# Kernel tuning notes

Hardware: AMD Instinct MI355X
Metric: run time of the kernel (lower is better)

## Reference

```python
import jax, jax.numpy as jnp
import numpy as np
import math

B, S, D, H = 2, 2048, 1024, 16
DK = D // H
EPS = 1e-6
TEMPERATURE = 1.0


def layernorm(x, a2, b2):
    # torch LayerNorm-variant: unbiased std (ddof=1), eps added to std
    mean = jnp.mean(x, axis=-1, keepdims=True)
    std = jnp.std(x, axis=-1, keepdims=True, ddof=1)
    return a2 * (x - mean) / (std + EPS) + b2


def setup_inputs() -> dict:
    key = jax.random.key(0)
    ks = jax.random.split(key, 12)
    scale = 1.0 / math.sqrt(D)
    inp = {
        "k": jax.random.normal(ks[0], (B, S, D), jnp.float32),
        "q": jax.random.normal(ks[1], (B, S, D), jnp.float32),
        "v": jax.random.normal(ks[2], (B, S, D), jnp.float32),
        "mask": jax.random.randint(ks[3], (B, S, S), 0, 2, jnp.int32),
        "Wq": jax.random.normal(ks[4], (D, D), jnp.float32) * scale,
        "bq": jnp.zeros((D,), jnp.float32),
        "Wk": jax.random.normal(ks[5], (D, D), jnp.float32) * scale,
        "bk": jnp.zeros((D,), jnp.float32),
        "Wv": jax.random.normal(ks[6], (D, D), jnp.float32) * scale,
        "bv": jnp.zeros((D,), jnp.float32),
        "Wo": jax.random.normal(ks[7], (D, D), jnp.float32) * scale,
        "bo": jnp.zeros((D,), jnp.float32),
        "a2": jnp.ones((D,), jnp.float32),
        "b2": jnp.zeros((D,), jnp.float32),
    }
    return inp


def reference(k, q, v, mask, Wq, bq, Wk, bk, Wv, bv, Wo, bo, a2, b2):
    # pre-norm all three streams
    kn = layernorm(k, a2, b2)
    qn = layernorm(q, a2, b2)
    vn = layernorm(v, a2, b2)
    # NOTE original quirk: linears[0](k)->query, linears[1](q)->key, linears[2](v)->value
    def proj(x, W, b):  # [B,S,D] -> [B,H,S,DK]
        y = x @ W + b
        return y.reshape(B, S, H, DK).transpose(0, 2, 1, 3)
    query = proj(kn, Wq, bq)
    key_ = proj(qn, Wk, bk)
    value = proj(vn, Wv, bv)
    scores = jnp.einsum('bhqd,bhkd->bhqk', query, key_) / math.sqrt(DK)
    scores = jnp.where(mask[:, None, :, :] == 0, jnp.float32(-1e9), scores)
    p_attn = jax.nn.softmax(scores * TEMPERATURE, axis=-1)
    x = jnp.einsum('bhqk,bhkd->bhqd', p_attn, value)
    x = x.transpose(0, 2, 1, 3).reshape(B, S, D)
    return x @ Wo + bo + vn  # residual adds normalized v
```

## Files before the change

kernel.cpp:

```cpp
#include <hip/hip_runtime.h>
#include <hip/hip_bf16.h>

#define B_  2
#define S_  2048
#define D_  1024
#define H_  16
#define DK_ 64
#define M_  4096

using bf16x8 = __attribute__((ext_vector_type(8))) __bf16;
using f32x4  = __attribute__((ext_vector_type(4))) float;

typedef __attribute__((address_space(1))) void gvoid;
typedef __attribute__((address_space(3))) void lvoid;

__device__ __forceinline__ void gload_lds16(const void* g, void* l) {
  __builtin_amdgcn_global_load_lds((gvoid*)g, (lvoid*)l, 16, 0, 0);
}

__device__ __forceinline__ f32x4 mfma16(bf16x8 a, bf16x8 b, f32x4 c) {
  return __builtin_amdgcn_mfma_f32_16x16x32_bf16(a, b, c, 0, 0, 0);
}

__device__ __forceinline__ int swz64(int row, int ce) {
  return row * 64 + ((((ce >> 3) ^ (row & 7)) << 3) | (ce & 7));
}

__global__ __launch_bounds__(256) void ln3_kernel(
    const float* __restrict__ kin, const float* __restrict__ qin,
    const float* __restrict__ vin,
    const float* __restrict__ a2, const float* __restrict__ b2,
    __hip_bfloat16* __restrict__ kn, __hip_bfloat16* __restrict__ qn,
    __hip_bfloat16* __restrict__ vnb, float* __restrict__ vnf)
{
  const int row = blockIdx.x;
  const int st  = blockIdx.y;
  const float* src = (st == 0) ? kin : (st == 1) ? qin : vin;
  const int t = threadIdx.x;
  const size_t base = (size_t)row * D_;

  float4 x = *(const float4*)(src + base + t * 4);
  float s  = x.x + x.y + x.z + x.w;
  float s2 = x.x * x.x + x.y * x.y + x.z * x.z + x.w * x.w;
  #pragma unroll
  for (int off = 32; off >= 1; off >>= 1) {
    s  += __shfl_down(s,  off, 64);
    s2 += __shfl_down(s2, off, 64);
  }
  __shared__ float red[4][2];
  __shared__ float stats[2];
  const int wid = t >> 6, lane = t & 63;
  if (lane == 0) { red[wid][0] = s; red[wid][1] = s2; }
  __syncthreads();
  if (t == 0) {
    float S  = red[0][0] + red[1][0] + red[2][0] + red[3][0];
    float S2 = red[0][1] + red[1][1] + red[2][1] + red[3][1];
    float mean = S * (1.0f / D_);
    float var  = fmaxf((S2 - S * mean) * (1.0f / (D_ - 1)), 0.0f);
    stats[0] = mean;
    stats[1] = 1.0f / (sqrtf(var) + 1e-6f);
  }
  __syncthreads();
  const float mean = stats[0], inv = stats[1];
  float4 ga = *(const float4*)(a2 + t * 4);
  float4 gb = *(const float4*)(b2 + t * 4);
  float o0 = ga.x * (x.x - mean) * inv + gb.x;
  float o1 = ga.y * (x.y - mean) * inv + gb.y;
  float o2 = ga.z * (x.z - mean) * inv + gb.z;
  float o3 = ga.w * (x.w - mean) * inv + gb.w;
  __hip_bfloat16* dst = (st == 0) ? kn : (st == 1) ? qn : vnb;
  union { __hip_bfloat16 h[4]; ushort4 u; } pk;
  pk.h[0] = __float2bfloat16(o0); pk.h[1] = __float2bfloat16(o1);
  pk.h[2] = __float2bfloat16(o2); pk.h[3] = __float2bfloat16(o3);
  *reinterpret_cast<ushort4*>((unsigned short*)dst + base + t * 4) = pk.u;
  if (st == 2) {
    float4 of = make_float4(o0, o1, o2, o3);
    *reinterpret_cast<float4*>(vnf + base + t * 4) = of;
  }
}

__global__ __launch_bounds__(256) void pack_mask_kernel(
    const int* __restrict__ mask, unsigned int* __restrict__ bits)
{
  const int w = blockIdx.x * 256 + threadIdx.x;
  const int* src = mask + (size_t)w * 32;
  unsigned int acc = 0;
  #pragma unroll
  for (int j = 0; j < 32; j += 4) {
    int4 t = *(const int4*)(src + j);
    acc |= (t.x != 0 ? 1u : 0u) << (j + 0);
    acc |= (t.y != 0 ? 1u : 0u) << (j + 1);
    acc |= (t.z != 0 ? 1u : 0u) << (j + 2);
    acc |= (t.w != 0 ? 1u : 0u) << (j + 3);
  }
  bits[w] = acc;
}

__global__ __launch_bounds__(256) void wt_cast_kernel(
    const float* __restrict__ W0, const float* __restrict__ W1,
    const float* __restrict__ W2, const float* __restrict__ W3,
    __hip_bfloat16* __restrict__ T0, __hip_bfloat16* __restrict__ T1,
    __hip_bfloat16* __restrict__ T2, __hip_bfloat16* __restrict__ T3)
{
  const int z = blockIdx.z;
  const float* W = (z == 0) ? W0 : (z == 1) ? W1 : (z == 2) ? W2 : W3;
  __hip_bfloat16* T = (z == 0) ? T0 : (z == 1) ? T1 : (z == 2) ? T2 : T3;
  __shared__ float tile[32][33];
  const int k0 = blockIdx.y * 32, n0 = blockIdx.x * 32;
  const int tx = threadIdx.x & 31, ty = threadIdx.x >> 5;
  #pragma unroll
  for (int i = ty; i < 32; i += 8)
    tile[i][tx] = W[(size_t)(k0 + i) * D_ + n0 + tx];
  __syncthreads();
  #pragma unroll
  for (int i = ty; i < 32; i += 8)
    T[(size_t)(n0 + i) * D_ + k0 + tx] = __float2bfloat16(tile[tx][i]);
}

__global__ __launch_bounds__(256) void proj3_kernel(
    const __hip_bfloat16* __restrict__ kn, const __hip_bfloat16* __restrict__ qn,
    const __hip_bfloat16* __restrict__ vnb,
    const __hip_bfloat16* __restrict__ Wqt, const __hip_bfloat16* __restrict__ Wkt,
    const __hip_bfloat16* __restrict__ Wvt,
    const float* __restrict__ bq, const float* __restrict__ bk,
    const float* __restrict__ bv,
    __hip_bfloat16* __restrict__ Qb, __hip_bfloat16* __restrict__ Kb,
    __hip_bfloat16* __restrict__ Vtb)
{
  const int z = blockIdx.z;
  const __hip_bfloat16* A  = (z == 0) ? kn  : (z == 1) ? qn  : vnb;
  const __hip_bfloat16* Wt = (z == 0) ? Wqt : (z == 1) ? Wkt : Wvt;
  const float* bias = (z == 0) ? bq : (z == 1) ? bk : bv;
  const float scale = (z == 0) ? 0.125f : 1.0f;

  __shared__ __hip_bfloat16 As[128 * 32];
  __shared__ __hip_bfloat16 Bs[128 * 32];
  const int n0 = blockIdx.x * 128;
  const int m0 = blockIdx.y * 128;
  const int tid = threadIdx.x;
  const int wid = tid >> 6, lane = tid & 63;
  const int wm = wid >> 1, wn = wid & 1;
  const int srow = lane >> 2;
  const int scol = (lane & 3) * 8;
  const int fr = lane & 15, fk8 = (lane >> 4) * 8, fq = lane >> 4;

  f32x4 acc[4][4] = {};

  for (int kt = 0; kt < D_ / 32; ++kt) {
    const int k0 = kt * 32;
    #pragma unroll
    for (int p = 0; p < 2; ++p) {
      const int r0 = 32 * wid + 16 * p;
      gload_lds16(A  + (size_t)(m0 + r0 + srow) * D_ + k0 + scol, &As[r0 * 32]);
      gload_lds16(Wt + (size_t)(n0 + r0 + srow) * D_ + k0 + scol, &Bs[r0 * 32]);
    }
    __syncthreads();
    bf16x8 af[4], bfr[4];
    #pragma unroll
    for (int i = 0; i < 4; ++i)
      af[i] = *(const bf16x8*)&As[(64 * wm + 16 * i + fr) * 32 + fk8];
    #pragma unroll
    for (int j = 0; j < 4; ++j)
      bfr[j] = *(const bf16x8*)&Bs[(64 * wn + 16 * j + fr) * 32 + fk8];
    #pragma unroll
    for (int i = 0; i < 4; ++i)
      #pragma unroll
      for (int j = 0; j < 4; ++j)
        acc[i][j] = mfma16(af[i], bfr[j], acc[i][j]);
    __syncthreads();
  }

  #pragma unroll
  for (int i = 0; i < 4; ++i) {
    #pragma unroll
    for (int j = 0; j < 4; ++j) {
      const int n = n0 + 64 * wn + 16 * j + fr;
      const float bn = bias[n];
      const int h = n >> 6, d = n & (DK_ - 1);
      #pragma unroll
      for (int r = 0; r < 4; ++r) {
        const int m = m0 + 64 * wm + 16 * i + 4 * fq + r;
        const int b = m >> 11, sl = m & (S_ - 1);
        const float val = (acc[i][j][r] + bn) * scale;
        if (z < 2) {
          __hip_bfloat16* dst = (z == 0) ? Qb : Kb;
          dst[((size_t)(b * H_ + h) * S_ + sl) * DK_ + d] = __float2bfloat16(val);
        } else {
          Vtb[((size_t)(b * H_ + h) * DK_ + d) * S_ + sl] = __float2bfloat16(val);
        }
      }
    }
  }
}

__global__ __launch_bounds__(256) void gemm_out_kernel(
    const __hip_bfloat16* __restrict__ A,
    const __hip_bfloat16* __restrict__ Wt,
    const float* __restrict__ bias,
    const float* __restrict__ residf,
    float* __restrict__ dst)
{
  __shared__ __hip_bfloat16 As[128 * 32];
  __shared__ __hip_bfloat16 Bs[128 * 32];
  const int n0 = blockIdx.x * 128;
  const int m0 = blockIdx.y * 128;
  const int tid = threadIdx.x;
  const int wid = tid >> 6, lane = tid & 63;
  const int wm = wid >> 1, wn = wid & 1;
  const int srow = lane >> 2;
  const int scol = (lane & 3) * 8;
  const int fr = lane & 15, fk8 = (lane >> 4) * 8, fq = lane >> 4;

  f32x4 acc[4][4] = {};

  for (int kt = 0; kt < D_ / 32; ++kt) {
    const int k0 = kt * 32;
    #pragma unroll
    for (int p = 0; p < 2; ++p) {
      const int r0 = 32 * wid + 16 * p;
      gload_lds16(A  + (size_t)(m0 + r0 + srow) * D_ + k0 + scol, &As[r0 * 32]);
      gload_lds16(Wt + (size_t)(n0 + r0 + srow) * D_ + k0 + scol, &Bs[r0 * 32]);
    }
    __syncthreads();
    bf16x8 af[4], bfr[4];
    #pragma unroll
    for (int i = 0; i < 4; ++i)
      af[i] = *(const bf16x8*)&As[(64 * wm + 16 * i + fr) * 32 + fk8];
    #pragma unroll
    for (int j = 0; j < 4; ++j)
      bfr[j] = *(const bf16x8*)&Bs[(64 * wn + 16 * j + fr) * 32 + fk8];
    #pragma unroll
    for (int i = 0; i < 4; ++i)
      #pragma unroll
      for (int j = 0; j < 4; ++j)
        acc[i][j] = mfma16(af[i], bfr[j], acc[i][j]);
    __syncthreads();
  }

  #pragma unroll
  for (int i = 0; i < 4; ++i) {
    #pragma unroll
    for (int j = 0; j < 4; ++j) {
      const int n = n0 + 64 * wn + 16 * j + fr;
      const float bn = bias[n];
      #pragma unroll
      for (int r = 0; r < 4; ++r) {
        const int m = m0 + 64 * wm + 16 * i + 4 * fq + r;
        dst[(size_t)m * D_ + n] =
            acc[i][j][r] + bn + residf[(size_t)m * D_ + n];
      }
    }
  }
}

__global__ __launch_bounds__(256) void attn_kernel(
    const __hip_bfloat16* __restrict__ Qb,
    const __hip_bfloat16* __restrict__ Kb,
    const __hip_bfloat16* __restrict__ Vtb,
    const unsigned int* __restrict__ mbits,
    __hip_bfloat16* __restrict__ Ob)
{
  __shared__ __hip_bfloat16 Ks[64 * 64];
  __shared__ __hip_bfloat16 Vs[64 * 64];
  __shared__ __hip_bfloat16 Ps[4][16 * 64];

  const int q0 = blockIdx.x * 64;
  const int bh = blockIdx.y;
  const int b = bh >> 4;
  const int h = bh & 15;
  const int tid = threadIdx.x, wid = tid >> 6, lane = tid & 63;
  const __hip_bfloat16* qp = Qb  + (size_t)bh * S_ * DK_;
  const __hip_bfloat16* kp = Kb  + (size_t)bh * S_ * DK_;
  const __hip_bfloat16* vp = Vtb + (size_t)bh * DK_ * S_;

  const int srow = lane >> 3;
  const int scol = ((lane & 7) ^ (lane >> 3)) << 3;
  const int fr = lane & 15, fq = lane >> 4, fk8 = fq * 8;

  const unsigned int* mrow = mbits + (size_t)b * S_ * (S_ / 32)
                           + (size_t)(q0 + 16 * wid + 4 * fq) * (S_ / 32);

  bf16x8 aq[2];
  #pragma unroll
  for (int ks = 0; ks < 2; ++ks)
    aq[ks] = *(const bf16x8*)(qp + (size_t)(q0 + 16 * wid + fr) * DK_
                                 + ks * 32 + fk8);

  float lrun[4] = {0.0f, 0.0f, 0.0f, 0.0f};
  f32x4 acc[4] = {};

  for (int kt = 0; kt < S_ / 64; ++kt) {
    const int k0 = kt * 64;
    #pragma unroll
    for (int p = 0; p < 2; ++p) {
      const int r0 = 16 * wid + 8 * p;
      gload_lds16(kp + (size_t)(k0 + r0 + srow) * DK_ + scol, &Ks[r0 * 64]);
      gload_lds16(vp + (size_t)(r0 + srow) * S_ + k0 + scol,  &Vs[r0 * 64]);
    }
    __syncthreads();

    f32x4 sf[4] = {};
    __builtin_amdgcn_s_setprio(1);
    #pragma unroll
    for (int ks = 0; ks < 2; ++ks) {
      #pragma unroll
      for (int ni = 0; ni < 4; ++ni) {
        const bf16x8 bk = *(const bf16x8*)&Ks[swz64(16 * ni + fr, ks * 32 + fk8)];
        sf[ni] = mfma16(aq[ks], bk, sf[ni]);
      }
    }
    __builtin_amdgcn_s_setprio(0);

    unsigned int wm0[4], wm1[4];
    #pragma unroll
    for (int r = 0; r < 4; ++r) {
      wm0[r] = mrow[(size_t)r * (S_ / 32) + 2 * kt];
      wm1[r] = mrow[(size_t)r * (S_ / 32) + 2 * kt + 1];
    }
    #pragma unroll
    for (int ni = 0; ni < 4; ++ni) {
      const int c = 16 * ni + fr;
      #pragma unroll
      for (int r = 0; r < 4; ++r) {
        float p = __expf(sf[ni][r]);
        const unsigned int bit = (((c < 32) ? wm0[r] : wm1[r]) >> (c & 31)) & 1u;
        p = bit ? p : 0.0f;
        lrun[r] += p;
        Ps[wid][swz64(4 * fq + r, c)] = __float2bfloat16(p);
      }
    }

    __builtin_amdgcn_s_setprio(1);
    #pragma unroll
    for (int ks = 0; ks < 2; ++ks) {
      const bf16x8 ap = *(const bf16x8*)&Ps[wid][swz64(fr, ks * 32 + fk8)];
      #pragma unroll
      for (int di = 0; di < 4; ++di) {
        const bf16x8 bv = *(const bf16x8*)&Vs[swz64(16 * di + fr, ks * 32 + fk8)];
        acc[di] = mfma16(ap, bv, acc[di]);
      }
    }
    __builtin_amdgcn_s_setprio(0);
    __syncthreads();
  }

  #pragma unroll
  for (int off = 1; off < 16; off <<= 1)
    #pragma unroll
    for (int r = 0; r < 4; ++r)
      lrun[r] += __shfl_xor(lrun[r], off, 64);

  #pragma unroll
  for (int di = 0; di < 4; ++di)
    #pragma unroll
    for (int r = 0; r < 4; ++r) {
      const int qg = q0 + 16 * wid + 4 * fq + r;
      Ob[((size_t)b * S_ + qg) * D_ + h * DK_ + 16 * di + fr] =
          __float2bfloat16(acc[di][r] / lrun[r]);
    }
}

extern "C" void kernel_launch(void* const* d_in, const int* in_sizes, int n_in,
                              void* d_out, int out_size, void* d_ws, size_t ws_size,
                              hipStream_t stream)
{
  const float* k    = (const float*)d_in[0];
  const float* q    = (const float*)d_in[1];
  const float* v    = (const float*)d_in[2];
  const int*   mask = (const int*)  d_in[3];
  const float* Wq   = (const float*)d_in[4];
  const float* bq   = (const float*)d_in[5];
  const float* Wk   = (const float*)d_in[6];
  const float* bk   = (const float*)d_in[7];
  const float* Wv   = (const float*)d_in[8];
  const float* bv   = (const float*)d_in[9];
  const float* Wo   = (const float*)d_in[10];
  const float* bo   = (const float*)d_in[11];
  const float* a2   = (const float*)d_in[12];
  const float* b2   = (const float*)d_in[13];

  char* ws = (char*)d_ws;
  const size_t MB = (size_t)1 << 20;
  __hip_bfloat16* kn   = (__hip_bfloat16*)(ws + 0 * MB);
  __hip_bfloat16* qn   = (__hip_bfloat16*)(ws + 8 * MB);
  __hip_bfloat16* vnb  = (__hip_bfloat16*)(ws + 16 * MB);
  __hip_bfloat16* Wqt  = (__hip_bfloat16*)(ws + 24 * MB);
  __hip_bfloat16* Wkt  = (__hip_bfloat16*)(ws + 26 * MB);
  __hip_bfloat16* Wvt  = (__hip_bfloat16*)(ws + 28 * MB);
  __hip_bfloat16* Wot  = (__hip_bfloat16*)(ws + 30 * MB);
  __hip_bfloat16* Qb   = (__hip_bfloat16*)(ws + 32 * MB);
  __hip_bfloat16* Kb   = (__hip_bfloat16*)(ws + 40 * MB);
  __hip_bfloat16* Vtb  = (__hip_bfloat16*)(ws + 48 * MB);
  __hip_bfloat16* Ob   = (__hip_bfloat16*)(ws + 56 * MB);
  unsigned int*   mbts = (unsigned int*)  (ws + 64 * MB);
  float*          vnf  = (float*)         (ws + 66 * MB);

  ln3_kernel<<<dim3(M_, 3), 256, 0, stream>>>(k, q, v, a2, b2, kn, qn, vnb, vnf);
  pack_mask_kernel<<<dim3(B_ * S_ * (S_ / 32) / 256), 256, 0, stream>>>(mask, mbts);
  wt_cast_kernel<<<dim3(32, 32, 4), 256, 0, stream>>>(Wq, Wk, Wv, Wo, Wqt, Wkt, Wvt, Wot);

  proj3_kernel<<<dim3(8, 32, 3), 256, 0, stream>>>(
      kn, qn, vnb, Wqt, Wkt, Wvt, bq, bk, bv, Qb, Kb, Vtb);

  attn_kernel<<<dim3(S_ / 64, B_ * H_), 256, 0, stream>>>(Qb, Kb, Vtb, mbts, Ob);

  gemm_out_kernel<<<dim3(8, 32), 256, 0, stream>>>(Ob, Wot, bo, vnf, (float*)d_out);
}
```

Baseline: 299.4 us.

## Widen GEMM K-tile to 64, halve output GEMM M-tile, use bf16 residual

Both projection and output GEMMs now stage 64-wide K slices in LDS, which halves the number of barrier-separated iterations. The output GEMM uses 64-row M tiles so it launches twice as many blocks and fills more CUs. The fp32 normalized-v buffer is dropped and the residual is read from the existing bf16 copy, cutting write and read traffic. The cost is a slight precision loss in the residual term and more LDS per block.

Measured after the change: 307.9 us. +2.8%, slower.

```diff
diff --git a/kernel.cpp b/kernel.cpp
--- a/kernel.cpp
+++ b/kernel.cpp
@@ -31,7 +31,7 @@
     const float* __restrict__ vin,
     const float* __restrict__ a2, const float* __restrict__ b2,
     __hip_bfloat16* __restrict__ kn, __hip_bfloat16* __restrict__ qn,
-    __hip_bfloat16* __restrict__ vnb, float* __restrict__ vnf)
+    __hip_bfloat16* __restrict__ vnb)
 {
   const int row = blockIdx.x;
   const int st  = blockIdx.y;
@@ -73,10 +73,6 @@
   pk.h[0] = __float2bfloat16(o0); pk.h[1] = __float2bfloat16(o1);
   pk.h[2] = __float2bfloat16(o2); pk.h[3] = __float2bfloat16(o3);
   *reinterpret_cast<ushort4*>((unsigned short*)dst + base + t * 4) = pk.u;
-  if (st == 2) {
-    float4 of = make_float4(o0, o1, o2, o3);
-    *reinterpret_cast<float4*>(vnf + base + t * 4) = of;
-  }
 }
 
 __global__ __launch_bounds__(256) void pack_mask_kernel(
@@ -133,40 +129,43 @@
   const float* bias = (z == 0) ? bq : (z == 1) ? bk : bv;
   const float scale = (z == 0) ? 0.125f : 1.0f;
 
-  __shared__ __hip_bfloat16 As[128 * 32];
-  __shared__ __hip_bfloat16 Bs[128 * 32];
+  __shared__ __hip_bfloat16 As[128 * 64];
+  __shared__ __hip_bfloat16 Bs[128 * 64];
   const int n0 = blockIdx.x * 128;
   const int m0 = blockIdx.y * 128;
   const int tid = threadIdx.x;
   const int wid = tid >> 6, lane = tid & 63;
   const int wm = wid >> 1, wn = wid & 1;
-  const int srow = lane >> 2;
-  const int scol = (lane & 3) * 8;
+  const int srow = lane >> 3;
+  const int scol = (lane & 7) * 8;
   const int fr = lane & 15, fk8 = (lane >> 4) * 8, fq = lane >> 4;
 
   f32x4 acc[4][4] = {};
 
-  for (int kt = 0; kt < D_ / 32; ++kt) {
-    const int k0 = kt * 32;
-    #pragma unroll
-    for (int p = 0; p < 2; ++p) {
-      const int r0 = 32 * wid + 16 * p;
-      gload_lds16(A  + (size_t)(m0 + r0 + srow) * D_ + k0 + scol, &As[r0 * 32]);
-      gload_lds16(Wt + (size_t)(n0 + r0 + srow) * D_ + k0 + scol, &Bs[r0 * 32]);
-    }
-    __syncthreads();
-    bf16x8 af[4], bfr[4];
-    #pragma unroll
-    for (int i = 0; i < 4; ++i)
-      af[i] = *(const bf16x8*)&As[(64 * wm + 16 * i + fr) * 32 + fk8];
-    #pragma unroll
-    for (int j = 0; j < 4; ++j)
-      bfr[j] = *(const bf16x8*)&Bs[(64 * wn + 16 * j + fr) * 32 + fk8];
-    #pragma unroll
-    for (int i = 0; i < 4; ++i)
+  for (int kt = 0; kt < D_ / 64; ++kt) {
+    const int k0 = kt * 64;
+    #pragma unroll
+    for (int p = 0; p < 4; ++p) {
+      const int r0 = 8 * wid + 32 * p;
+      gload_lds16(A  + (size_t)(m0 + r0 + srow) * D_ + k0 + scol, &As[r0 * 64]);
+      gload_lds16(Wt + (size_t)(n0 + r0 + srow) * D_ + k0 + scol, &Bs[r0 * 64]);
+    }
+    __syncthreads();
+    #pragma unroll
+    for (int ks = 0; ks < 2; ++ks) {
+      bf16x8 af[4], bfr[4];
+      #pragma unroll
+      for (int i = 0; i < 4; ++i)
+        af[i] = *(const bf16x8*)&As[(64 * wm + 16 * i + fr) * 64 + ks * 32 + fk8];
       #pragma unroll
       for (int j = 0; j < 4; ++j)
-        acc[i][j] = mfma16(af[i], bfr[j], acc[i][j]);
+        bfr[j] = *(const bf16x8*)&Bs[(64 * wn + 16 * j + fr) * 64 + ks * 32 + fk8];
+      #pragma unroll
+      for (int i = 0; i < 4; ++i)
+        #pragma unroll
+        for (int j = 0; j < 4; ++j)
+          acc[i][j] = mfma16(af[i], bfr[j], acc[i][j]);
+    }
     __syncthreads();
   }
 
@@ -197,57 +196,64 @@
     const __hip_bfloat16* __restrict__ A,
     const __hip_bfloat16* __restrict__ Wt,
     const float* __restrict__ bias,
-    const float* __restrict__ residf,
+    const __hip_bfloat16* __restrict__ residb,
     float* __restrict__ dst)
 {
-  __shared__ __hip_bfloat16 As[128 * 32];
-  __shared__ __hip_bfloat16 Bs[128 * 32];
+  __shared__ __hip_bfloat16 As[64 * 64];
+  __shared__ __hip_bfloat16 Bs[128 * 64];
   const int n0 = blockIdx.x * 128;
-  const int m0 = blockIdx.y * 128;
+  const int m0 = blockIdx.y * 64;
   const int tid = threadIdx.x;
   const int wid = tid >> 6, lane = tid & 63;
   const int wm = wid >> 1, wn = wid & 1;
-  const int srow = lane >> 2;
-  const int scol = (lane & 3) * 8;
+  const int srow = lane >> 3;
+  const int scol = (lane & 7) * 8;
   const int fr = lane & 15, fk8 = (lane >> 4) * 8, fq = lane >> 4;
 
-  f32x4 acc[4][4] = {};
-
-  for (int kt = 0; kt < D_ / 32; ++kt) {
-    const int k0 = kt * 32;
+  f32x4 acc[2][4] = {};
+
+  for (int kt = 0; kt < D_ / 64; ++kt) {
+    const int k0 = kt * 64;
     #pragma unroll
     for (int p = 0; p < 2; ++p) {
-      const int r0 = 32 * wid + 16 * p;
-      gload_lds16(A  + (size_t)(m0 + r0 + srow) * D_ + k0 + scol, &As[r0 * 32]);
-      gload_lds16(Wt + (size_t)(n0 + r0 + srow) * D_ + k0 + scol, &Bs[r0 * 32]);
-    }
-    __syncthreads();
-    bf16x8 af[4], bfr[4];
-    #pragma unroll
-    for (int i = 0; i < 4; ++i)
-      af[i] = *(const bf16x8*)&As[(64 * wm + 16 * i + fr) * 32 + fk8];
-    #pragma unroll
-    for (int j = 0; j < 4; ++j)
-      bfr[j] = *(const bf16x8*)&Bs[(64 * wn + 16 * j + fr) * 32 + fk8];
-    #pragma unroll
-    for (int i = 0; i < 4; ++i)
+      const int r0 = 8 * wid + 32 * p;
+      gload_lds16(A + (size_t)(m0 + r0 + srow) * D_ + k0 + scol, &As[r0 * 64]);
+    }
+    #pragma unroll
+    for (int p = 0; p < 4; ++p) {
+      const int r0 = 8 * wid + 32 * p;
+      gload_lds16(Wt + (size_t)(n0 + r0 + srow) * D_ + k0 + scol, &Bs[r0 * 64]);
+    }
+    __syncthreads();
+    #pragma unroll
+    for (int ks = 0; ks < 2; ++ks) {
+      bf16x8 af[2], bfr[4];
+      #pragma unroll
+      for (int i = 0; i < 2; ++i)
+        af[i] = *(const bf16x8*)&As[(32 * wm + 16 * i + fr) * 64 + ks * 32 + fk8];
       #pragma unroll
       for (int j = 0; j < 4; ++j)
-        acc[i][j] = mfma16(af[i], bfr[j], acc[i][j]);
-    __syncthreads();
-  }
-
-  #pragma unroll
-  for (int i = 0; i < 4; ++i) {
+        bfr[j] = *(const bf16x8*)&Bs[(64 * wn + 16 * j + fr) * 64 + ks * 32 + fk8];
+      #pragma unroll
+      for (int i = 0; i < 2; ++i)
+        #pragma unroll
+        for (int j = 0; j < 4; ++j)
+          acc[i][j] = mfma16(af[i], bfr[j], acc[i][j]);
+    }
+    __syncthreads();
+  }
+
+  #pragma unroll
+  for (int i = 0; i < 2; ++i) {
     #pragma unroll
     for (int j = 0; j < 4; ++j) {
       const int n = n0 + 64 * wn + 16 * j + fr;
       const float bn = bias[n];
       #pragma unroll
       for (int r = 0; r < 4; ++r) {
-        const int m = m0 + 64 * wm + 16 * i + 4 * fq + r;
-        dst[(size_t)m * D_ + n] =
-            acc[i][j][r] + bn + residf[(size_t)m * D_ + n];
+        const int m = m0 + 32 * wm + 16 * i + 4 * fq + r;
+        dst[(size_t)m * D_ + n] = acc[i][j][r] + bn
+            + __bfloat162float(residb[(size_t)m * D_ + n]);
       }
     }
   }
@@ -393,9 +399,8 @@
   __hip_bfloat16* Vtb  = (__hip_bfloat16*)(ws + 48 * MB);
   __hip_bfloat16* Ob   = (__hip_bfloat16*)(ws + 56 * MB);
   unsigned int*   mbts = (unsigned int*)  (ws + 64 * MB);
-  float*          vnf  = (float*)         (ws + 66 * MB);
-
-  ln3_kernel<<<dim3(M_, 3), 256, 0, stream>>>(k, q, v, a2, b2, kn, qn, vnb, vnf);
+
+  ln3_kernel<<<dim3(M_, 3), 256, 0, stream>>>(k, q, v, a2, b2, kn, qn, vnb);
   pack_mask_kernel<<<dim3(B_ * S_ * (S_ / 32) / 256), 256, 0, stream>>>(mask, mbts);
   wt_cast_kernel<<<dim3(32, 32, 4), 256, 0, stream>>>(Wq, Wk, Wv, Wo, Wqt, Wkt, Wvt, Wot);
 
@@ -404,5 +409,5 @@
 
   attn_kernel<<<dim3(S_ / 64, B_ * H_), 256, 0, stream>>>(Qb, Kb, Vtb, mbts, Ob);
 
-  gemm_out_kernel<<<dim3(8, 32), 256, 0, stream>>>(Ob, Wot, bo, vnf, (float*)d_out);
-}
+  gemm_out_kernel<<<dim3(8, 64), 256, 0, stream>>>(Ob, Wot, bo, vnb, (float*)d_out);
+}
```
